# Kernel tuning notes

Measured on AMD Instinct MI355X. Metric: run time of the kernel, lower is better.

Reference implementation:

```python
import jax, jax.numpy as jnp
import numpy as np

N_NODES = 100000
N_EDGES = 600000
D_IN = 128
D_HID = 128
D_OUT = 64


def setup_inputs() -> dict:
    key = jax.random.key(0)
    ks = jax.random.split(key, 6)
    x = jax.random.normal(ks[0], (N_NODES, D_IN), dtype=jnp.float32)
    edge_index = jax.random.randint(ks[1], (2, N_EDGES), 0, N_NODES, dtype=jnp.int32)
    # Glorot-ish init for GCNConv weights
    W1 = jax.random.normal(ks[2], (D_IN, D_HID), dtype=jnp.float32) * (1.0 / np.sqrt(D_IN))
    W2 = jax.random.normal(ks[3], (D_HID, D_HID), dtype=jnp.float32) * (1.0 / np.sqrt(D_HID))
    W3 = jax.random.normal(ks[4], (D_HID, D_OUT), dtype=jnp.float32) * (1.0 / np.sqrt(D_HID))
    b1 = jnp.zeros((D_HID,), dtype=jnp.float32)
    b2 = jnp.zeros((D_HID,), dtype=jnp.float32)
    b3 = jnp.zeros((D_OUT,), dtype=jnp.float32)
    return {"x": x, "edge_index": edge_index, "W1": W1, "b1": b1,
            "W2": W2, "b2": b2, "W3": W3, "b3": b3}


def reference(x, edge_index, W1, b1, W2, b2, W3, b3):
    N = x.shape[0]
    # PyG GCNConv default: add self-loops, symmetric degree normalization.
    row, col = edge_index[0], edge_index[1]
    loops = jnp.arange(N, dtype=row.dtype)
    row = jnp.concatenate([row, loops])  # source nodes
    col = jnp.concatenate([col, loops])  # destination nodes (aggregation target)
    deg = jax.ops.segment_sum(jnp.ones(row.shape, dtype=x.dtype), col, num_segments=N)
    dinv = jax.lax.rsqrt(jnp.maximum(deg, 1.0))  # deg >= 1 due to self-loops
    norm = dinv[row] * dinv[col]  # [E+N]

    def gcn_conv(h, W, b):
        hw = h @ W                                   # dense transform [N, D]
        msg = hw[row] * norm[:, None]                # gather + normalize [E+N, D]
        return jax.ops.segment_sum(msg, col, num_segments=N) + b  # scatter-add

    h = jax.nn.relu(gcn_conv(x, W1, b1))
    # dropout p=0.5 is identity in eval mode (training=False)
    h = jax.nn.relu(gcn_conv(h, W2, b2))
    h = gcn_conv(h, W3, b3)
    return jax.nn.log_softmax(h, axis=1)
```

## Files before the change

### kernel.cpp

```cpp
#include <hip/hip_runtime.h>

#define NN 100000
#define NE 600000

typedef unsigned short u16;
typedef float f32x4 __attribute__((ext_vector_type(4)));
typedef short s16x8 __attribute__((ext_vector_type(8)));

__device__ inline u16 f2bf(float f) {
    unsigned u = __float_as_uint(f);
    return (u16)((u + 0x7FFFu + ((u >> 16) & 1u)) >> 16);
}
__device__ inline float bflo(unsigned u) { return __uint_as_float(u << 16); }
__device__ inline float bfhi(unsigned u) { return __uint_as_float(u & 0xFFFF0000u); }
__device__ inline unsigned pk(float a, float b) {
    return (unsigned)f2bf(a) | ((unsigned)f2bf(b) << 16);
}


__global__ void k_init_deg(int* __restrict__ deg, int n) {
    int i = blockIdx.x * 256 + threadIdx.x;
    if (i < n) deg[i] = 0;
}

__global__ void k_deg_count(const int* __restrict__ col, int* __restrict__ deg, int E) {
    int e = blockIdx.x * 256 + threadIdx.x;
    if (e < E) atomicAdd(&deg[col[e]], 1);
}

__global__ void k_dinv(const int* __restrict__ deg, float* __restrict__ dinv, int n) {
    int i = blockIdx.x * 256 + threadIdx.x;
    if (i < n) dinv[i] = rsqrtf((float)(deg[i] + 1));
}

__global__ void k_scan1(const int* __restrict__ deg, int* __restrict__ offs,
                        int* __restrict__ bsums, int n) {
    __shared__ int s[256];
    int t = threadIdx.x;
    int i = blockIdx.x * 256 + t;
    int v = (i < n) ? deg[i] : 0;
    s[t] = v;
    __syncthreads();
    for (int off = 1; off < 256; off <<= 1) {
        int x = (t >= off) ? s[t - off] : 0;
        __syncthreads();
        s[t] += x;
        __syncthreads();
    }
    if (i < n) offs[i] = s[t] - v;
    if (t == 255) bsums[blockIdx.x] = s[255];
}

__global__ void k_scan2(int* __restrict__ bsums, int nb) {
    __shared__ int s[512];
    int t = threadIdx.x;
    int v = (t < nb) ? bsums[t] : 0;
    s[t] = v;
    __syncthreads();
    for (int off = 1; off < 512; off <<= 1) {
        int x = (t >= off) ? s[t - off] : 0;
        __syncthreads();
        s[t] += x;
        __syncthreads();
    }
    if (t < nb) bsums[t] = s[t] - v;
}

__global__ void k_scan3(int* __restrict__ offs, const int* __restrict__ bsums,
                        int* __restrict__ cursor, int n) {
    int i = blockIdx.x * 256 + threadIdx.x;
    if (i < n) {
        int o = offs[i] + bsums[i >> 8];
        offs[i] = o;
        cursor[i] = o;
    }
}

__global__ void k_fill(const int* __restrict__ row, const int* __restrict__ col,
                       int* __restrict__ cursor, int* __restrict__ srcs, int E) {
    int e = blockIdx.x * 256 + threadIdx.x;
    if (e < E) {
        int p = atomicAdd(&cursor[col[e]], 1);
        srcs[p] = row[e];
    }
}


template <int DOUT>
__global__ __launch_bounds__(256)
void k_pack_w(const float* __restrict__ W, u16* __restrict__ Wp) {
    int gid = blockIdx.x * 256 + threadIdx.x;
    if (gid >= DOUT * 128) return;
    int i  = gid & 7;
    int l  = (gid >> 3) & 63;
    int kk = (gid >> 9) & 3;
    int t  = gid >> 11;
    int k = kk * 32 + ((l >> 4) << 3) + i;
    int c = t * 16 + (l & 15);
    Wp[gid] = f2bf(W[k * DOUT + c]);
}


template <int DOUT, bool OB16, bool AF32>
__global__ __launch_bounds__(256)
void k_gemm_mfma(const void* __restrict__ Hin, const u16* __restrict__ Wp,
                 const float* __restrict__ dinv, void* __restrict__ Gout, int n) {
    constexpr int NT = DOUT / 16;
    int tid = threadIdx.x;
    int w = tid >> 6, l = tid & 63;
    int r0 = blockIdx.x * 64 + w * 16;
    int arow = r0 + (l & 15);
    bool avalid = arow < n;
    const s16x8* Arow = (const s16x8*)((const u16*)Hin + (size_t)arow * 128);
    const float* Arow32 = (const float*)Hin + (size_t)arow * 128;
    const s16x8* Wp8 = (const s16x8*)Wp;
    const s16x8 zero = {0, 0, 0, 0, 0, 0, 0, 0};

    f32x4 acc[NT];
#pragma unroll
    for (int t = 0; t < NT; t++) acc[t] = {0.f, 0.f, 0.f, 0.f};

#pragma unroll
    for (int kk = 0; kk < 4; kk++) {
        s16x8 a;
        if (AF32) {
            if (avalid) {
                const f32x4* p = (const f32x4*)(Arow32 + kk * 32 + ((l >> 4) << 3));
                f32x4 f0 = p[0], f1 = p[1];
                a[0] = (short)f2bf(f0[0]); a[1] = (short)f2bf(f0[1]);
                a[2] = (short)f2bf(f0[2]); a[3] = (short)f2bf(f0[3]);
                a[4] = (short)f2bf(f1[0]); a[5] = (short)f2bf(f1[1]);
                a[6] = (short)f2bf(f1[2]); a[7] = (short)f2bf(f1[3]);
            } else a = zero;
        } else {
            a = avalid ? Arow[kk * 4 + (l >> 4)] : zero;
        }
#pragma unroll
        for (int t = 0; t < NT; t++) {
            s16x8 b = Wp8[(t * 4 + kk) * 64 + l];
            acc[t] = __builtin_amdgcn_mfma_f32_16x16x32_bf16(a, b, acc[t], 0, 0, 0);
        }
    }

    int col = l & 15;
#pragma unroll
    for (int r = 0; r < 4; r++) {
        int gr = r0 + (l >> 4) * 4 + r;
        if (gr < n) {
            float di = dinv[gr];
#pragma unroll
            for (int t = 0; t < NT; t++) {
                float v = acc[t][r] * di;
                if (OB16)
                    ((u16*)Gout)[(size_t)gr * DOUT + t * 16 + col] = f2bf(v);
                else
                    ((float*)Gout)[(size_t)gr * DOUT + t * 16 + col] = v;
            }
        }
    }
}


#define ACC8(A, U) \
    A[0] += bflo(U.x); A[1] += bfhi(U.x); A[2] += bflo(U.y); A[3] += bfhi(U.y); \
    A[4] += bflo(U.z); A[5] += bfhi(U.z); A[6] += bflo(U.w); A[7] += bfhi(U.w);

__global__ __launch_bounds__(256)
void k_agg_relu(const uint4* __restrict__ G, const int* __restrict__ offs,
                const int* __restrict__ deg, const int* __restrict__ srcs,
                const float* __restrict__ dinv, const float* __restrict__ bias,
                uint4* __restrict__ out, int n) {
    int t = blockIdx.x * 256 + threadIdx.x;
    int wv = t >> 6;
    int lane = t & 63;
    int hl = lane & 15;
    int node = wv * 4 + (lane >> 4);
    if (node >= n) return;

    uint4 us = G[(size_t)node * 16 + hl];
    float a0[8], a1[8], a2[8], a3[8];
    a0[0] = bflo(us.x); a0[1] = bfhi(us.x); a0[2] = bflo(us.y); a0[3] = bfhi(us.y);
    a0[4] = bflo(us.z); a0[5] = bfhi(us.z); a0[6] = bflo(us.w); a0[7] = bfhi(us.w);
#pragma unroll
    for (int i = 0; i < 8; i++) { a1[i] = 0.f; a2[i] = 0.f; a3[i] = 0.f; }

    int start = offs[node];
    int cnt = deg[node];
    int j = 0;
    for (; j + 4 <= cnt; j += 4) {
        int s0 = srcs[start + j + 0];
        int s1 = srcs[start + j + 1];
        int s2 = srcs[start + j + 2];
        int s3 = srcs[start + j + 3];
        uint4 u0 = G[(size_t)s0 * 16 + hl];
        uint4 u1 = G[(size_t)s1 * 16 + hl];
        uint4 u2 = G[(size_t)s2 * 16 + hl];
        uint4 u3 = G[(size_t)s3 * 16 + hl];
        ACC8(a0, u0) ACC8(a1, u1) ACC8(a2, u2) ACC8(a3, u3)
    }
    for (; j < cnt; j++) {
        int s = srcs[start + j];
        uint4 u = G[(size_t)s * 16 + hl];
        ACC8(a0, u)
    }

    float di = dinv[node];
    const float4* b8 = (const float4*)bias;
    float4 b0 = b8[hl * 2], b1 = b8[hl * 2 + 1];
    float bb[8] = {b0.x, b0.y, b0.z, b0.w, b1.x, b1.y, b1.z, b1.w};
    float r[8];
#pragma unroll
    for (int i = 0; i < 8; i++) {
        float s = (a0[i] + a1[i]) + (a2[i] + a3[i]);
        r[i] = fmaxf(fmaf(s, di, bb[i]), 0.f);
    }
    out[(size_t)node * 16 + hl] =
        make_uint4(pk(r[0], r[1]), pk(r[2], r[3]), pk(r[4], r[5]), pk(r[6], r[7]));
}

#define ACC4(A, U) \
    A[0] += bflo(U.x); A[1] += bfhi(U.x); A[2] += bflo(U.y); A[3] += bfhi(U.y);

__global__ __launch_bounds__(256)
void k_agg_softmax(const uint2* __restrict__ G, const int* __restrict__ offs,
                   const int* __restrict__ deg, const int* __restrict__ srcs,
                   const float* __restrict__ dinv, const float* __restrict__ bias,
                   float4* __restrict__ out, int n) {
    int t = blockIdx.x * 256 + threadIdx.x;
    int wv = t >> 6;
    int lane = t & 63;
    int hl = lane & 15;
    int node = wv * 4 + (lane >> 4);
    if (node >= n) return;

    uint2 us = G[(size_t)node * 16 + hl];
    float a0[4], a1[4], a2[4], a3[4];
    a0[0] = bflo(us.x); a0[1] = bfhi(us.x); a0[2] = bflo(us.y); a0[3] = bfhi(us.y);
#pragma unroll
    for (int i = 0; i < 4; i++) { a1[i] = 0.f; a2[i] = 0.f; a3[i] = 0.f; }

    int start = offs[node];
    int cnt = deg[node];
    int j = 0;
    for (; j + 4 <= cnt; j += 4) {
        int s0 = srcs[start + j + 0];
        int s1 = srcs[start + j + 1];
        int s2 = srcs[start + j + 2];
        int s3 = srcs[start + j + 3];
        uint2 u0 = G[(size_t)s0 * 16 + hl];
        uint2 u1 = G[(size_t)s1 * 16 + hl];
        uint2 u2 = G[(size_t)s2 * 16 + hl];
        uint2 u3 = G[(size_t)s3 * 16 + hl];
        ACC4(a0, u0) ACC4(a1, u1) ACC4(a2, u2) ACC4(a3, u3)
    }
    for (; j < cnt; j++) {
        int s = srcs[start + j];
        uint2 u = G[(size_t)s * 16 + hl];
        ACC4(a0, u)
    }

    float di = dinv[node];
    float4 bb = ((const float4*)bias)[hl];
    float t0 = fmaf((a0[0] + a1[0]) + (a2[0] + a3[0]), di, bb.x);
    float t1 = fmaf((a0[1] + a1[1]) + (a2[1] + a3[1]), di, bb.y);
    float t2 = fmaf((a0[2] + a1[2]) + (a2[2] + a3[2]), di, bb.z);
    float t3 = fmaf((a0[3] + a1[3]) + (a2[3] + a3[3]), di, bb.w);
    float m = fmaxf(fmaxf(t0, t1), fmaxf(t2, t3));
#pragma unroll
    for (int off = 1; off < 16; off <<= 1) m = fmaxf(m, __shfl_xor(m, off, 64));
    float e = expf(t0 - m) + expf(t1 - m) + expf(t2 - m) + expf(t3 - m);
#pragma unroll
    for (int off = 1; off < 16; off <<= 1) e += __shfl_xor(e, off, 64);
    float lse = m + logf(e);
    out[(size_t)node * 16 + hl] = make_float4(t0 - lse, t1 - lse, t2 - lse, t3 - lse);
}


extern "C" void kernel_launch(void* const* d_in, const int* in_sizes, int n_in,
                              void* d_out, int out_size, void* d_ws, size_t ws_size,
                              hipStream_t stream) {
    const float* x  = (const float*)d_in[0];
    const int*   ei = (const int*)d_in[1];
    const int*   row = ei;
    const int*   col = ei + NE;
    const float* W1 = (const float*)d_in[2];
    const float* b1 = (const float*)d_in[3];
    const float* W2 = (const float*)d_in[4];
    const float* b2 = (const float*)d_in[5];
    const float* W3 = (const float*)d_in[6];
    const float* b3 = (const float*)d_in[7];
    float* outp = (float*)d_out;

    char* ws = (char*)d_ws;
    size_t off = 0;
    auto alloc = [&](size_t bytes) -> void* {
        void* p = (void*)(ws + off);
        off += (bytes + 255) & ~(size_t)255;
        return p;
    };
    float* dinv  = (float*)alloc((size_t)NN * 4);
    float* bufA  = (float*)alloc((size_t)NN * 128 * 4);
    u16*   bufB  = (u16*)alloc((size_t)NN * 128 * 2);
    int*   deg   = (int*)alloc((size_t)NN * 4);
    int*   offs  = (int*)alloc((size_t)NN * 4);
    int*   cursor= (int*)alloc((size_t)NN * 4);
    int*   bsums = (int*)alloc(1024 * 4);
    int*   srcs  = (int*)alloc((size_t)NE * 4);
    u16*   wp1   = (u16*)alloc(128 * 128 * 2);
    u16*   wp2   = (u16*)alloc(128 * 128 * 2);
    u16*   wp3   = (u16*)alloc(128 * 64 * 2);

    int nbN = (NN + 255) / 256;
    int nbE = (NE + 255) / 256;

    k_init_deg <<<nbN, 256, 0, stream>>>(deg, NN);
    k_deg_count<<<nbE, 256, 0, stream>>>(col, deg, NE);
    k_dinv     <<<nbN, 256, 0, stream>>>(deg, dinv, NN);
    k_scan1    <<<nbN, 256, 0, stream>>>(deg, offs, bsums, NN);
    k_scan2    <<<1,   512, 0, stream>>>(bsums, nbN);
    k_scan3    <<<nbN, 256, 0, stream>>>(offs, bsums, cursor, NN);
    k_fill     <<<nbE, 256, 0, stream>>>(row, col, cursor, srcs, NE);

    k_pack_w<128><<<64, 256, 0, stream>>>(W1, wp1);
    k_pack_w<128><<<64, 256, 0, stream>>>(W2, wp2);
    k_pack_w<64> <<<32, 256, 0, stream>>>(W3, wp3);

    int gb = (NN + 63) / 64;
    int ab4 = ((NN + 3) / 4 * 64 + 255) / 256;

    k_gemm_mfma<128, true, true><<<gb, 256, 0, stream>>>(x, wp1, dinv, bufA, NN);
    k_agg_relu <<<ab4, 256, 0, stream>>>((uint4*)bufA, offs, deg, srcs, dinv, b1, (uint4*)bufB, NN);
    k_gemm_mfma<128, true, false><<<gb, 256, 0, stream>>>(bufB, wp2, dinv, bufA, NN);
    k_agg_relu <<<ab4, 256, 0, stream>>>((uint4*)bufA, offs, deg, srcs, dinv, b2, (uint4*)bufB, NN);
    k_gemm_mfma<64, true, false><<<gb, 256, 0, stream>>>(bufB, wp3, dinv, bufA, NN);
    k_agg_softmax<<<ab4, 256, 0, stream>>>((uint2*)bufA, offs, deg, srcs, dinv, b3, (float4*)outp, NN);
}
```

Measured before the change: 307.1 us.

## Bin nodes by degree for balanced aggregation, fuse prep kernels, double GEMM rows

Adds a degree histogram and counting-sort pass that builds a node order grouped by in-degree. The aggregation kernels then process nodes in that order, so the four nodes sharing a wavefront have similar edge counts and less divergence. The change also folds the dinv computation into the scan, merges the three weight-pack kernels into one, and has each GEMM wave compute 32 rows instead of 16. The cost is two extra small kernels, an extra indirection in aggregation, and scattered output writes, since neighbouring lanes now handle unrelated node IDs.

```diff
diff --git a/kernel.cpp b/kernel.cpp
--- a/kernel.cpp
+++ b/kernel.cpp
@@ -18,9 +18,10 @@
 }
 
 
-__global__ void k_init_deg(int* __restrict__ deg, int n) {
+__global__ void k_init_deg(int* __restrict__ deg, int* __restrict__ hist, int n) {
     int i = blockIdx.x * 256 + threadIdx.x;
     if (i < n) deg[i] = 0;
+    if (blockIdx.x == 0 && threadIdx.x < 64) hist[threadIdx.x] = 0;
 }
 
 __global__ void k_deg_count(const int* __restrict__ col, int* __restrict__ deg, int E) {
@@ -28,17 +29,17 @@
     if (e < E) atomicAdd(&deg[col[e]], 1);
 }
 
-__global__ void k_dinv(const int* __restrict__ deg, float* __restrict__ dinv, int n) {
-    int i = blockIdx.x * 256 + threadIdx.x;
-    if (i < n) dinv[i] = rsqrtf((float)(deg[i] + 1));
-}
-
 __global__ void k_scan1(const int* __restrict__ deg, int* __restrict__ offs,
-                        int* __restrict__ bsums, int n) {
+                        int* __restrict__ bsums, float* __restrict__ dinv,
+                        int* __restrict__ hist, int n) {
     __shared__ int s[256];
     int t = threadIdx.x;
     int i = blockIdx.x * 256 + t;
     int v = (i < n) ? deg[i] : 0;
+    if (i < n) {
+        dinv[i] = rsqrtf((float)(v + 1));
+        atomicAdd(&hist[v < 63 ? v : 63], 1);
+    }
     s[t] = v;
     __syncthreads();
     for (int off = 1; off < 256; off <<= 1) {
@@ -85,19 +86,49 @@
     }
 }
 
-
-template <int DOUT>
-__global__ __launch_bounds__(256)
-void k_pack_w(const float* __restrict__ W, u16* __restrict__ Wp) {
-    int gid = blockIdx.x * 256 + threadIdx.x;
-    if (gid >= DOUT * 128) return;
-    int i  = gid & 7;
-    int l  = (gid >> 3) & 63;
-    int kk = (gid >> 9) & 3;
-    int t  = gid >> 11;
+__global__ void k_scan_bins(const int* __restrict__ hist, int* __restrict__ bcur) {
+    __shared__ int s[64];
+    int t = threadIdx.x;
+    int v = hist[t];
+    s[t] = v;
+    __syncthreads();
+    for (int off = 1; off < 64; off <<= 1) {
+        int x = (t >= off) ? s[t - off] : 0;
+        __syncthreads();
+        s[t] += x;
+        __syncthreads();
+    }
+    bcur[t] = s[t] - v;
+}
+
+__global__ void k_scatter_nodes(const int* __restrict__ deg, int* __restrict__ bcur,
+                                int* __restrict__ order, int n) {
+    int i = blockIdx.x * 256 + threadIdx.x;
+    if (i < n) {
+        int b = deg[i]; b = b < 63 ? b : 63;
+        order[atomicAdd(&bcur[b], 1)] = i;
+    }
+}
+
+
+__device__ inline void pack_one(const float* W, u16* Wp, int g, int DOUT) {
+    int i  = g & 7;
+    int l  = (g >> 3) & 63;
+    int kk = (g >> 9) & 3;
+    int t  = g >> 11;
     int k = kk * 32 + ((l >> 4) << 3) + i;
     int c = t * 16 + (l & 15);
-    Wp[gid] = f2bf(W[k * DOUT + c]);
+    Wp[g] = f2bf(W[k * DOUT + c]);
+}
+
+__global__ __launch_bounds__(256)
+void k_pack_all(const float* __restrict__ W1, const float* __restrict__ W2,
+                const float* __restrict__ W3, u16* __restrict__ wp1,
+                u16* __restrict__ wp2, u16* __restrict__ wp3) {
+    int gid = blockIdx.x * 256 + threadIdx.x;
+    if (gid < 16384) pack_one(W1, wp1, gid, 128);
+    else if (gid < 32768) pack_one(W2, wp2, gid - 16384, 128);
+    else if (gid < 40960) pack_one(W3, wp3, gid - 32768, 64);
 }
 
 
@@ -108,53 +139,75 @@
     constexpr int NT = DOUT / 16;
     int tid = threadIdx.x;
     int w = tid >> 6, l = tid & 63;
-    int r0 = blockIdx.x * 64 + w * 16;
-    int arow = r0 + (l & 15);
-    bool avalid = arow < n;
-    const s16x8* Arow = (const s16x8*)((const u16*)Hin + (size_t)arow * 128);
-    const float* Arow32 = (const float*)Hin + (size_t)arow * 128;
+    int r0 = blockIdx.x * 128 + w * 32;
+    int arow0 = r0 + (l & 15);
+    int arow1 = arow0 + 16;
+    bool av0 = arow0 < n, av1 = arow1 < n;
+    const s16x8* A0 = (const s16x8*)((const u16*)Hin + (size_t)arow0 * 128);
+    const s16x8* A1 = (const s16x8*)((const u16*)Hin + (size_t)arow1 * 128);
+    const float* A032 = (const float*)Hin + (size_t)arow0 * 128;
+    const float* A132 = (const float*)Hin + (size_t)arow1 * 128;
     const s16x8* Wp8 = (const s16x8*)Wp;
     const s16x8 zero = {0, 0, 0, 0, 0, 0, 0, 0};
 
-    f32x4 acc[NT];
-#pragma unroll
-    for (int t = 0; t < NT; t++) acc[t] = {0.f, 0.f, 0.f, 0.f};
+    f32x4 acc0[NT], acc1[NT];
+#pragma unroll
+    for (int t = 0; t < NT; t++) { acc0[t] = {0.f,0.f,0.f,0.f}; acc1[t] = {0.f,0.f,0.f,0.f}; }
 
 #pragma unroll
     for (int kk = 0; kk < 4; kk++) {
-        s16x8 a;
+        s16x8 a0, a1;
         if (AF32) {
-            if (avalid) {
-                const f32x4* p = (const f32x4*)(Arow32 + kk * 32 + ((l >> 4) << 3));
+            a0 = zero; a1 = zero;
+            if (av0) {
+                const f32x4* p = (const f32x4*)(A032 + kk * 32 + ((l >> 4) << 3));
                 f32x4 f0 = p[0], f1 = p[1];
-                a[0] = (short)f2bf(f0[0]); a[1] = (short)f2bf(f0[1]);
-                a[2] = (short)f2bf(f0[2]); a[3] = (short)f2bf(f0[3]);
-                a[4] = (short)f2bf(f1[0]); a[5] = (short)f2bf(f1[1]);
-                a[6] = (short)f2bf(f1[2]); a[7] = (short)f2bf(f1[3]);
-            } else a = zero;
+                a0[0]=(short)f2bf(f0[0]); a0[1]=(short)f2bf(f0[1]);
+                a0[2]=(short)f2bf(f0[2]); a0[3]=(short)f2bf(f0[3]);
+                a0[4]=(short)f2bf(f1[0]); a0[5]=(short)f2bf(f1[1]);
+                a0[6]=(short)f2bf(f1[2]); a0[7]=(short)f2bf(f1[3]);
+            }
+            if (av1) {
+                const f32x4* p = (const f32x4*)(A132 + kk * 32 + ((l >> 4) << 3));
+                f32x4 f0 = p[0], f1 = p[1];
+                a1[0]=(short)f2bf(f0[0]); a1[1]=(short)f2bf(f0[1]);
+                a1[2]=(short)f2bf(f0[2]); a1[3]=(short)f2bf(f0[3]);
+                a1[4]=(short)f2bf(f1[0]); a1[5]=(short)f2bf(f1[1]);
+                a1[6]=(short)f2bf(f1[2]); a1[7]=(short)f2bf(f1[3]);
+            }
         } else {
-            a = avalid ? Arow[kk * 4 + (l >> 4)] : zero;
+            a0 = av0 ? A0[kk * 4 + (l >> 4)] : zero;
+            a1 = av1 ? A1[kk * 4 + (l >> 4)] : zero;
         }
 #pragma unroll
         for (int t = 0; t < NT; t++) {
             s16x8 b = Wp8[(t * 4 + kk) * 64 + l];
-            acc[t] = __builtin_amdgcn_mfma_f32_16x16x32_bf16(a, b, acc[t], 0, 0, 0);
+            acc0[t] = __builtin_amdgcn_mfma_f32_16x16x32_bf16(a0, b, acc0[t], 0, 0, 0);
+            acc1[t] = __builtin_amdgcn_mfma_f32_16x16x32_bf16(a1, b, acc1[t], 0, 0, 0);
         }
     }
 
     int col = l & 15;
 #pragma unroll
     for (int r = 0; r < 4; r++) {
-        int gr = r0 + (l >> 4) * 4 + r;
-        if (gr < n) {
-            float di = dinv[gr];
+        int gr0 = r0 + (l >> 4) * 4 + r;
+        if (gr0 < n) {
+            float di = dinv[gr0];
 #pragma unroll
             for (int t = 0; t < NT; t++) {
-                float v = acc[t][r] * di;
-                if (OB16)
-                    ((u16*)Gout)[(size_t)gr * DOUT + t * 16 + col] = f2bf(v);
-                else
-                    ((float*)Gout)[(size_t)gr * DOUT + t * 16 + col] = v;
+                float v = acc0[t][r] * di;
+                if (OB16) ((u16*)Gout)[(size_t)gr0 * DOUT + t * 16 + col] = f2bf(v);
+                else      ((float*)Gout)[(size_t)gr0 * DOUT + t * 16 + col] = v;
+            }
+        }
+        int gr1 = gr0 + 16;
+        if (gr1 < n) {
+            float di = dinv[gr1];
+#pragma unroll
+            for (int t = 0; t < NT; t++) {
+                float v = acc1[t][r] * di;
+                if (OB16) ((u16*)Gout)[(size_t)gr1 * DOUT + t * 16 + col] = f2bf(v);
+                else      ((float*)Gout)[(size_t)gr1 * DOUT + t * 16 + col] = v;
             }
         }
     }
@@ -168,14 +221,16 @@
 __global__ __launch_bounds__(256)
 void k_agg_relu(const uint4* __restrict__ G, const int* __restrict__ offs,
                 const int* __restrict__ deg, const int* __restrict__ srcs,
+                const int* __restrict__ order,
                 const float* __restrict__ dinv, const float* __restrict__ bias,
                 uint4* __restrict__ out, int n) {
     int t = blockIdx.x * 256 + threadIdx.x;
     int wv = t >> 6;
     int lane = t & 63;
     int hl = lane & 15;
-    int node = wv * 4 + (lane >> 4);
-    if (node >= n) return;
+    int gnode = wv * 4 + (lane >> 4);
+    if (gnode >= n) return;
+    int node = order[gnode];
 
     uint4 us = G[(size_t)node * 16 + hl];
     float a0[8], a1[8], a2[8], a3[8];
@@ -224,14 +279,16 @@
 __global__ __launch_bounds__(256)
 void k_agg_softmax(const uint2* __restrict__ G, const int* __restrict__ offs,
                    const int* __restrict__ deg, const int* __restrict__ srcs,
+                   const int* __restrict__ order,
                    const float* __restrict__ dinv, const float* __restrict__ bias,
                    float4* __restrict__ out, int n) {
     int t = blockIdx.x * 256 + threadIdx.x;
     int wv = t >> 6;
     int lane = t & 63;
     int hl = lane & 15;
-    int node = wv * 4 + (lane >> 4);
-    if (node >= n) return;
+    int gnode = wv * 4 + (lane >> 4);
+    if (gnode >= n) return;
+    int node = order[gnode];
 
     uint2 us = G[(size_t)node * 16 + hl];
     float a0[4], a1[4], a2[4], a3[4];
@@ -305,6 +362,9 @@
     int*   offs  = (int*)alloc((size_t)NN * 4);
     int*   cursor= (int*)alloc((size_t)NN * 4);
     int*   bsums = (int*)alloc(1024 * 4);
+    int*   hist  = (int*)alloc(64 * 4);
+    int*   bcur  = (int*)alloc(64 * 4);
+    int*   order = (int*)alloc((size_t)NN * 4);
     int*   srcs  = (int*)alloc((size_t)NE * 4);
     u16*   wp1   = (u16*)alloc(128 * 128 * 2);
     u16*   wp2   = (u16*)alloc(128 * 128 * 2);
@@ -313,25 +373,23 @@
     int nbN = (NN + 255) / 256;
     int nbE = (NE + 255) / 256;
 
-    k_init_deg <<<nbN, 256, 0, stream>>>(deg, NN);
+    k_init_deg <<<nbN, 256, 0, stream>>>(deg, hist, NN);
     k_deg_count<<<nbE, 256, 0, stream>>>(col, deg, NE);
-    k_dinv     <<<nbN, 256, 0, stream>>>(deg, dinv, NN);
-    k_scan1    <<<nbN, 256, 0, stream>>>(deg, offs, bsums, NN);
+    k_scan1    <<<nbN, 256, 0, stream>>>(deg, offs, bsums, dinv, hist, NN);
     k_scan2    <<<1,   512, 0, stream>>>(bsums, nbN);
     k_scan3    <<<nbN, 256, 0, stream>>>(offs, bsums, cursor, NN);
     k_fill     <<<nbE, 256, 0, stream>>>(row, col, cursor, srcs, NE);
-
-    k_pack_w<128><<<64, 256, 0, stream>>>(W1, wp1);
-    k_pack_w<128><<<64, 256, 0, stream>>>(W2, wp2);
-    k_pack_w<64> <<<32, 256, 0, stream>>>(W3, wp3);
-
-    int gb = (NN + 63) / 64;
+    k_scan_bins<<<1,    64, 0, stream>>>(hist, bcur);
+    k_scatter_nodes<<<nbN, 256, 0, stream>>>(deg, bcur, order, NN);
+    k_pack_all <<<160, 256, 0, stream>>>(W1, W2, W3, wp1, wp2, wp3);
+
+    int gb = (NN + 127) / 128;
     int ab4 = ((NN + 3) / 4 * 64 + 255) / 256;
 
     k_gemm_mfma<128, true, true><<<gb, 256, 0, stream>>>(x, wp1, dinv, bufA, NN);
-    k_agg_relu <<<ab4, 256, 0, stream>>>((uint4*)bufA, offs, deg, srcs, dinv, b1, (uint4*)bufB, NN);
+    k_agg_relu <<<ab4, 256, 0, stream>>>((uint4*)bufA, offs, deg, srcs, order, dinv, b1, (uint4*)bufB, NN);
     k_gemm_mfma<128, true, false><<<gb, 256, 0, stream>>>(bufB, wp2, dinv, bufA, NN);
-    k_agg_relu <<<ab4, 256, 0, stream>>>((uint4*)bufA, offs, deg, srcs, dinv, b2, (uint4*)bufB, NN);
+    k_agg_relu <<<ab4, 256, 0, stream>>>((uint4*)bufA, offs, deg, srcs, order, dinv, b2, (uint4*)bufB, NN);
     k_gemm_mfma<64, true, false><<<gb, 256, 0, stream>>>(bufB, wp3, dinv, bufA, NN);
-    k_agg_softmax<<<ab4, 256, 0, stream>>>((uint2*)bufA, offs, deg, srcs, dinv, b3, (float4*)outp, NN);
-}
+    k_agg_softmax<<<ab4, 256, 0, stream>>>((uint2*)bufA, offs, deg, srcs, order, dinv, b3, (float4*)outp, NN);
+}
```

After: 1.044 ms. 240% more time.
